# Performance work log

Hardware: AMD Instinct MI355X
Metric: run time of the kernel (lower is better)

Reference implementation:

```python
import jax, jax.numpy as jnp
import numpy as np

N_NODES = 100_000
N_EDGES = 1_600_000
NEG_SLOPE = 0.2

# layer configs: (in_channels, heads, out_channels, has_proj)
LAYERS = [(193, 8, 16, True), (128, 8, 16, False), (128, 8, 16, False), (128, 8, 8, True)]


def _gat_params(key, fin, H, C):
    ks = jax.random.split(key, 6)
    s = 1.0 / np.sqrt(fin)
    Wl = jax.random.normal(ks[0], (fin, H * C), dtype=jnp.float32) * s
    bl = jax.random.normal(ks[1], (H * C,), dtype=jnp.float32) * 0.01
    Wr = jax.random.normal(ks[2], (fin, H * C), dtype=jnp.float32) * s
    br = jax.random.normal(ks[3], (H * C,), dtype=jnp.float32) * 0.01
    att = jax.random.normal(ks[4], (H, C), dtype=jnp.float32) * (1.0 / np.sqrt(C))
    bias = jax.random.normal(ks[5], (H * C,), dtype=jnp.float32) * 0.01
    return Wl, bl, Wr, br, att, bias


def setup_inputs() -> dict:
    key = jax.random.key(0)
    ks = jax.random.split(key, 16)
    inp = {}
    inp['x'] = jax.random.normal(ks[0], (N_NODES, 193), dtype=jnp.float32)
    inp['edge_index'] = jax.random.randint(ks[1], (2, N_EDGES), 0, N_NODES, dtype=jnp.int64)
    for li, (fin, H, C, _) in enumerate(LAYERS, start=1):
        Wl, bl, Wr, br, att, bias = _gat_params(ks[1 + li], fin, H, C)
        inp[f'Wl{li}'] = Wl; inp[f'bl{li}'] = bl
        inp[f'Wr{li}'] = Wr; inp[f'br{li}'] = br
        inp[f'att{li}'] = att; inp[f'bias{li}'] = bias
    # residual projections where in_channels != heads*out_channels
    inp['proj1_W'] = jax.random.normal(ks[8], (193, 128), dtype=jnp.float32) * (1.0 / np.sqrt(193))
    inp['proj1_b'] = jax.random.normal(ks[9], (128,), dtype=jnp.float32) * 0.01
    inp['proj4_W'] = jax.random.normal(ks[10], (128, 64), dtype=jnp.float32) * (1.0 / np.sqrt(128))
    inp['proj4_b'] = jax.random.normal(ks[11], (64,), dtype=jnp.float32) * 0.01
    inp['lin1_W'] = jax.random.normal(ks[12], (64, 32), dtype=jnp.float32) * (1.0 / np.sqrt(64))
    inp['lin1_b'] = jax.random.normal(ks[13], (32,), dtype=jnp.float32) * 0.01
    return inp


def _gatv2(x, src, dst, Wl, bl, Wr, br, att, bias):
    # x: [N, Fin]; att: [H, C]
    N = x.shape[0]
    H, C = att.shape
    xl = (x @ Wl + bl).reshape(N, H, C)  # source transform
    xr = (x @ Wr + br).reshape(N, H, C)  # destination transform
    m = xl[src] + xr[dst]                # [E, H, C] edge gather
    e = jnp.einsum('ehc,hc->eh', jax.nn.leaky_relu(m, NEG_SLOPE), att)  # [E, H]
    emax = jax.ops.segment_max(e, dst, num_segments=N)  # per-dst softmax max
    p = jnp.exp(e - emax[dst])
    denom = jax.ops.segment_sum(p, dst, num_segments=N)
    alpha = p / (denom[dst] + 1e-16)     # [E, H]
    out = jax.ops.segment_sum(alpha[:, :, None] * xl[src], dst, num_segments=N)  # [N, H, C]
    return out.reshape(N, H * C) + bias


def _forward(x, edge_index, params):
    src, dst = edge_index[0], edge_index[1]
    h = x
    for li in range(4):
        Wl, bl, Wr, br, att, bias, projW, projb = params[li]
        g = _gatv2(h, src, dst, Wl, bl, Wr, br, att, bias)
        res = h @ projW + projb if projW is not None else h
        h = jax.nn.gelu(g + res, approximate=False)
    Wf, bf = params[4]
    return h @ Wf + bf


def reference(x, edge_index,
              Wl1, bl1, Wr1, br1, att1, bias1,
              Wl2, bl2, Wr2, br2, att2, bias2,
              Wl3, bl3, Wr3, br3, att3, bias3,
              Wl4, bl4, Wr4, br4, att4, bias4,
              proj1_W, proj1_b, proj4_W, proj4_b, lin1_W, lin1_b):
    params = [
        (Wl1, bl1, Wr1, br1, att1, bias1, proj1_W, proj1_b),
        (Wl2, bl2, Wr2, br2, att2, bias2, None, None),
        (Wl3, bl3, Wr3, br3, att3, bias3, None, None),
        (Wl4, bl4, Wr4, br4, att4, bias4, proj4_W, proj4_b),
        (lin1_W, lin1_b),
    ]
    return _forward(x, edge_index, params)
```

## Files before the change

kernel.cpp:

```cpp
#include <hip/hip_runtime.h>
#include <hip/hip_bf16.h>

#define NNODES 100000

typedef short s16x8 __attribute__((ext_vector_type(8)));
typedef float f32x4 __attribute__((ext_vector_type(4)));

__device__ inline ushort f2bf(float f) {
    uint u = __float_as_uint(f);
    uint r = u + 0x7fffu + ((u >> 16) & 1u);
    return (ushort)(r >> 16);
}
__device__ inline float bf2f(ushort u) { return __uint_as_float(((uint)u) << 16); }
__device__ inline float bflo(uint u) { return __uint_as_float(u << 16); }
__device__ inline float bfhi(uint u) { return __uint_as_float(u & 0xffff0000u); }

__device__ inline void gl_lds16(const ushort* g, ushort* l) {
    __builtin_amdgcn_global_load_lds((const __attribute__((address_space(1))) void*)g,
                                     (__attribute__((address_space(3))) void*)l, 16, 0, 0);
}

__global__ void hist_kernel(const int* __restrict__ dst, int E, int* __restrict__ deg) {
    int e = blockIdx.x * blockDim.x + threadIdx.x;
    if (e < E) atomicAdd(&deg[dst[e]], 1);
}

__global__ __launch_bounds__(256) void scan_part(const int* __restrict__ deg,
                                                 int* __restrict__ bsum, int n) {
    int t = threadIdx.x;
    int base = blockIdx.x * 1024 + t * 4;
    int4 v = make_int4(0, 0, 0, 0);
    if (base + 3 < n) v = *(const int4*)(deg + base);
    else {
        if (base + 0 < n) v.x = deg[base + 0];
        if (base + 1 < n) v.y = deg[base + 1];
        if (base + 2 < n) v.z = deg[base + 2];
    }
    int s = v.x + v.y + v.z + v.w;
#pragma unroll
    for (int o = 1; o < 64; o <<= 1) s += __shfl_xor(s, o);
    __shared__ int ws[4];
    if ((t & 63) == 0) ws[t >> 6] = s;
    __syncthreads();
    if (t == 0) bsum[blockIdx.x] = ws[0] + ws[1] + ws[2] + ws[3];
}

__global__ __launch_bounds__(128) void scan_bsum(int* __restrict__ bsum, int nb,
                                                 int* __restrict__ rowptr, int n) {
    __shared__ int s[128];
    int t = threadIdx.x;
    int v = (t < nb) ? bsum[t] : 0;
    s[t] = v;
    __syncthreads();
#pragma unroll
    for (int o = 1; o < 128; o <<= 1) {
        int u = (t >= o) ? s[t - o] : 0;
        __syncthreads();
        s[t] += u;
        __syncthreads();
    }
    if (t < nb) bsum[t] = s[t] - v;
    if (t == 127) rowptr[n] = s[127];
}

__global__ __launch_bounds__(256) void scan_apply(const int* __restrict__ deg,
                                                  const int* __restrict__ bsum,
                                                  int* __restrict__ rowptr, int n) {
    int t = threadIdx.x;
    int base = blockIdx.x * 1024 + t * 4;
    int4 v = make_int4(0, 0, 0, 0);
    if (base + 3 < n) v = *(const int4*)(deg + base);
    else {
        if (base + 0 < n) v.x = deg[base + 0];
        if (base + 1 < n) v.y = deg[base + 1];
        if (base + 2 < n) v.z = deg[base + 2];
    }
    int s = v.x + v.y + v.z + v.w;
    int lane = t & 63, w = t >> 6;
    int incl = s;
#pragma unroll
    for (int o = 1; o < 64; o <<= 1) {
        int u = __shfl_up(incl, o);
        if (lane >= o) incl += u;
    }
    __shared__ int wsum[4];
    if (lane == 63) wsum[w] = incl;
    __syncthreads();
    int woff = 0;
    if (w > 0) woff += wsum[0];
    if (w > 1) woff += wsum[1];
    if (w > 2) woff += wsum[2];
    int off = bsum[blockIdx.x] + woff + (incl - s);
    int4 r;
    r.x = off;
    r.y = off + v.x;
    r.z = r.y + v.y;
    r.w = r.z + v.z;
    if (base + 3 < n) *(int4*)(rowptr + base) = r;
    else {
        if (base + 0 < n) rowptr[base + 0] = r.x;
        if (base + 1 < n) rowptr[base + 1] = r.y;
        if (base + 2 < n) rowptr[base + 2] = r.z;
    }
}

__global__ void scatter_kernel(const int* __restrict__ src, const int* __restrict__ dst, int E,
                               const int* __restrict__ rowptr, int* __restrict__ cursor,
                               int* __restrict__ csr) {
    int e = blockIdx.x * blockDim.x + threadIdx.x;
    if (e < E) {
        int d = dst[e];
        int pos = rowptr[d] + atomicAdd(&cursor[d], 1);
        csr[pos] = src[e];
    }
}

struct WConvDesc { const float* W; ushort* Wt; int K, N, Kp; };
struct WConvArgs { WConvDesc d[10]; };

__global__ void convert_weights(WConvArgs args) {
    WConvDesc dd = args.d[blockIdx.y];
    int total = dd.N * dd.Kp;
    for (int i = blockIdx.x * 256 + threadIdx.x; i < total; i += gridDim.x * 256) {
        int n = i / dd.Kp, k = i - n * dd.Kp;
        float v = (k < dd.K) ? dd.W[(size_t)k * dd.N + n] : 0.f;
        dd.Wt[i] = f2bf(v);
    }
}

struct BCat { const float* src; float* dst; int len; };
struct BCatArgs { BCat d[10]; };
__global__ void concat_bias(BCatArgs a) {
    BCat dd = a.d[blockIdx.x];
    for (int i = threadIdx.x; i < dd.len; i += 256) dd.dst[i] = dd.src[i];
}

__global__ void convert_x(const float* __restrict__ x, ushort* __restrict__ xb, int M) {
    int total = M * 56;
    for (int i = blockIdx.x * 256 + threadIdx.x; i < total; i += gridDim.x * 256) {
        int n = i / 56;
        int k4 = (i - n * 56) * 4;
        ushort o[4];
#pragma unroll
        for (int j = 0; j < 4; ++j) {
            int k = k4 + j;
            o[j] = (k < 193) ? f2bf(x[(size_t)n * 193 + k]) : (ushort)0;
        }
        *(uint2*)(xb + (size_t)n * 224 + k4) = *(const uint2*)o;
    }
}

template <int BN>
__global__ __launch_bounds__(256) void gemm_mfma(const ushort* __restrict__ A,
                                                 const ushort* __restrict__ BtAll,
                                                 const float* __restrict__ biasAll,
                                                 ushort* __restrict__ C,
                                                 int M, int Kp, int Cstride) {
    const int col0 = blockIdx.y * BN;
    const ushort* Bt = BtAll + (size_t)col0 * Kp;
    const float* bias = biasAll + col0;

    __shared__ ushort As[128 * 32];
    __shared__ ushort Bs[BN * 32];
    const int t = threadIdx.x;
    const int r0 = blockIdx.x * 128;
    const int lane = t & 63;
    const int w = t >> 6;
    const int la = lane & 15;
    const int lk = (lane >> 4) * 8;

    constexpr int MR = (BN == 128) ? 4 : 2;
    const int m0 = (BN == 128) ? (w >> 1) * 64 : w * 32;
    const int n0 = (BN == 128) ? (w & 1) * 64 : 0;

    f32x4 acc[MR][4];
#pragma unroll
    for (int i = 0; i < MR; ++i)
#pragma unroll
        for (int j = 0; j < 4; ++j) acc[i][j] = (f32x4)0.f;

    const int lrow4 = lane >> 2;
    const int lkq = (lane & 3) * 8;
    const int arow0 = min(r0 + (2 * w) * 16 + lrow4, M - 1);
    const int arow1 = min(r0 + (2 * w + 1) * 16 + lrow4, M - 1);
    const size_t aoff0 = (size_t)arow0 * Kp + lkq;
    const size_t aoff1 = (size_t)arow1 * Kp + lkq;
    const int brow0 = (BN == 128) ? (2 * w) * 16 + lrow4 : w * 16 + lrow4;
    const int brow1 = (2 * w + 1) * 16 + lrow4;
    const size_t boff0 = (size_t)brow0 * Kp + lkq;
    const size_t boff1 = (size_t)brow1 * Kp + lkq;

    for (int k0 = 0; k0 < Kp; k0 += 32) {
        gl_lds16(A + aoff0 + k0, &As[(2 * w) * 512]);
        gl_lds16(A + aoff1 + k0, &As[(2 * w + 1) * 512]);
        if (BN == 128) {
            gl_lds16(Bt + boff0 + k0, &Bs[(2 * w) * 512]);
            gl_lds16(Bt + boff1 + k0, &Bs[(2 * w + 1) * 512]);
        } else {
            gl_lds16(Bt + boff0 + k0, &Bs[w * 512]);
        }
        asm volatile("s_waitcnt vmcnt(0)" ::: "memory");
        __syncthreads();
        s16x8 av[MR], bv[4];
#pragma unroll
        for (int i = 0; i < MR; ++i)
            av[i] = *(const s16x8*)&As[(m0 + i * 16 + la) * 32 + lk];
#pragma unroll
        for (int j = 0; j < 4; ++j)
            bv[j] = *(const s16x8*)&Bs[(n0 + j * 16 + la) * 32 + lk];
#pragma unroll
        for (int i = 0; i < MR; ++i)
#pragma unroll
            for (int j = 0; j < 4; ++j)
                acc[i][j] = __builtin_amdgcn_mfma_f32_16x16x32_bf16(av[i], bv[j], acc[i][j], 0, 0, 0);
        __syncthreads();
    }
    const int lrow = (lane >> 4) * 4;
#pragma unroll
    for (int i = 0; i < MR; ++i) {
#pragma unroll
        for (int j = 0; j < 4; ++j) {
            int col = n0 + j * 16 + la;
            float bval = bias[col];
#pragma unroll
            for (int r = 0; r < 4; ++r) {
                int row = r0 + m0 + i * 16 + lrow + r;
                if (row < M) C[(size_t)row * Cstride + col0 + col] = f2bf(acc[i][j][r] + bval);
            }
        }
    }
}

template <int HC>
__global__ __launch_bounds__(256) void gat_agg(const ushort* __restrict__ xcat, int xstride,
                                               int xr_off,
                                               const ushort* __restrict__ res, int rstride, int roff,
                                               const float* __restrict__ att,
                                               const float* __restrict__ bias,
                                               const int* __restrict__ rowptr,
                                               const int* __restrict__ csr,
                                               float* __restrict__ hout, int hstride,
                                               ushort* __restrict__ houtb, int M) {
    constexpr int LPE = HC / 8;
    constexpr int EPI = 64 / LPE;
    constexpr int QSH = (HC == 128) ? 4 : 3;
    const int n = blockIdx.x * 4 + (threadIdx.x >> 6);
    if (n >= M) return;
    const int lane = threadIdx.x & 63;
    const int clane = lane & (LPE - 1);
    const int q = lane >> QSH;

    const char* xb = (const char*)xcat;
    const uint xrowB = (uint)xstride * 2u;
    const uint chB = (uint)clane * 16u;

    float xr[8], at[8];
    {
        uint4 u = *(const uint4*)(xb + (uint)n * xrowB + (uint)xr_off * 2u + chB);
        xr[0] = bflo(u.x); xr[1] = bfhi(u.x); xr[2] = bflo(u.y); xr[3] = bfhi(u.y);
        xr[4] = bflo(u.z); xr[5] = bfhi(u.z); xr[6] = bflo(u.w); xr[7] = bfhi(u.w);
        const float L2E = 1.4426950408889634f;
        float4 a0 = *(const float4*)(att + 8 * clane);
        float4 a1 = *(const float4*)(att + 8 * clane + 4);
        at[0] = a0.x * L2E; at[1] = a0.y * L2E; at[2] = a0.z * L2E; at[3] = a0.w * L2E;
        at[4] = a1.x * L2E; at[5] = a1.y * L2E; at[6] = a1.z * L2E; at[7] = a1.w * L2E;
    }

    const int s0 = rowptr[n], s1 = rowptr[n + 1];
    float ssum = 0.f;
    float acc[8] = {0.f, 0.f, 0.f, 0.f, 0.f, 0.f, 0.f, 0.f};

    if (s1 > s0) {
        const int nq = (s1 - s0 + EPI - 1) >> (6 - QSH);
        auto ISSUE = [&](uint4& buf, bool& val, int p) {
            if (p >= nq) { val = false; buf = make_uint4(0u, 0u, 0u, 0u); return; }
            int g = s0 + p * EPI + q;
            val = g < s1;
            int src = csr[min(g, s1 - 1)];
            buf = *(const uint4*)(xb + (uint)src * xrowB + chB);
        };
        auto COMPUTE = [&](const uint4& buf, bool val) {
            float x[8];
            x[0] = bflo(buf.x); x[1] = bfhi(buf.x); x[2] = bflo(buf.y); x[3] = bfhi(buf.y);
            x[4] = bflo(buf.z); x[5] = bfhi(buf.z); x[6] = bflo(buf.w); x[7] = bfhi(buf.w);
            float prod = 0.f;
#pragma unroll
            for (int j = 0; j < 8; ++j) {
                float v = x[j] + xr[j];
                float l = fmaxf(v, 0.2f * v);
                prod = fmaf(l, at[j], prod);
            }
            if constexpr (HC == 128) prod += __shfl_xor(prod, 1);
            float pe = val ? exp2f(prod) : 0.f;
            ssum += pe;
#pragma unroll
            for (int j = 0; j < 8; ++j) acc[j] = fmaf(pe, x[j], acc[j]);
        };
        uint4 b0, b1, b2, b3;
        bool v0, v1, v2, v3;
        ISSUE(b0, v0, 0); ISSUE(b1, v1, 1); ISSUE(b2, v2, 2); ISSUE(b3, v3, 3);
        for (int p = 0; p < nq; p += 4) {
            COMPUTE(b0, v0); ISSUE(b0, v0, p + 4);
            if (p + 1 < nq) { COMPUTE(b1, v1); ISSUE(b1, v1, p + 5); }
            if (p + 2 < nq) { COMPUTE(b2, v2); ISSUE(b2, v2, p + 6); }
            if (p + 3 < nq) { COMPUTE(b3, v3); ISSUE(b3, v3, p + 7); }
        }
    }

#pragma unroll
    for (int o = LPE; o < 64; o <<= 1) {
        ssum += __shfl_xor(ssum, o);
#pragma unroll
        for (int j = 0; j < 8; ++j) acc[j] += __shfl_xor(acc[j], o);
    }

    float inv = 1.f / (ssum + 1e-16f);
    if constexpr (HC == 128) {
        int ch = 8 * clane + 2 * q;
        float a0s = (q == 0) ? acc[0] : (q == 1) ? acc[2] : (q == 2) ? acc[4] : acc[6];
        float a1s = (q == 0) ? acc[1] : (q == 1) ? acc[3] : (q == 2) ? acc[5] : acc[7];
        uint u = *(const uint*)(res + (size_t)n * rstride + roff + ch);
        float r0v = bflo(u), r1v = bfhi(u);
        float2 b2 = *(const float2*)(bias + ch);
        float y0 = fmaf(a0s, inv, b2.x + r0v);
        float y1 = fmaf(a1s, inv, b2.y + r1v);
        float o0 = 0.5f * y0 * (1.f + erff(y0 * 0.70710678118654752f));
        float o1 = 0.5f * y1 * (1.f + erff(y1 * 0.70710678118654752f));
        if (hout) *(float2*)(hout + (size_t)n * hstride + ch) = make_float2(o0, o1);
        if (houtb) *(uint*)(houtb + (size_t)n * HC + ch) = (uint)f2bf(o0) | ((uint)f2bf(o1) << 16);
    } else {
        int ch = 8 * clane + q;
        float a0s = (q == 0) ? acc[0] : (q == 1) ? acc[1] : (q == 2) ? acc[2] : (q == 3) ? acc[3]
                  : (q == 4) ? acc[4] : (q == 5) ? acc[5] : (q == 6) ? acc[6] : acc[7];
        float r0v = bf2f(res[(size_t)n * rstride + roff + ch]);
        float y0 = fmaf(a0s, inv, bias[ch] + r0v);
        float o0 = 0.5f * y0 * (1.f + erff(y0 * 0.70710678118654752f));
        if (hout) hout[(size_t)n * hstride + ch] = o0;
        if (houtb) houtb[(size_t)n * HC + ch] = f2bf(o0);
    }
}

__global__ __launch_bounds__(256) void final_linear(const float* __restrict__ h,
                                                    const float* __restrict__ W,
                                                    const float* __restrict__ b,
                                                    float* __restrict__ out, int M) {
    __shared__ float Ws[64 * 32];
    __shared__ float bs[32];
    __shared__ float hs[8][64];
    int t = threadIdx.x;
    for (int i = t; i < 64 * 32; i += 256) Ws[i] = W[i];
    if (t < 32) bs[t] = b[t];
    int r0 = blockIdx.x * 8;
    for (int i = t; i < 8 * 64; i += 256) {
        int r = i >> 6, c = i & 63;
        hs[r][c] = (r0 + r < M) ? h[(size_t)(r0 + r) * 64 + c] : 0.f;
    }
    __syncthreads();
    int lr = t >> 5;
    int col = t & 31;
    int row = r0 + lr;
    if (row >= M) return;
    float acc = bs[col];
#pragma unroll 8
    for (int k = 0; k < 64; ++k) acc += hs[lr][k] * Ws[k * 32 + col];
    out[(size_t)row * 32 + col] = acc;
}

extern "C" void kernel_launch(void* const* d_in, const int* in_sizes, int n_in,
                              void* d_out, int out_size, void* d_ws, size_t ws_size,
                              hipStream_t stream) {
    const float* x = (const float*)d_in[0];
    const int* ei = (const int*)d_in[1];
    const int E = in_sizes[1] / 2;
    const int* srcp = ei;
    const int* dstp = ei + E;

    const float* Wl[4]  = {(const float*)d_in[2],  (const float*)d_in[8],  (const float*)d_in[14], (const float*)d_in[20]};
    const float* bl[4]  = {(const float*)d_in[3],  (const float*)d_in[9],  (const float*)d_in[15], (const float*)d_in[21]};
    const float* Wr[4]  = {(const float*)d_in[4],  (const float*)d_in[10], (const float*)d_in[16], (const float*)d_in[22]};
    const float* br[4]  = {(const float*)d_in[5],  (const float*)d_in[11], (const float*)d_in[17], (const float*)d_in[23]};
    const float* att[4] = {(const float*)d_in[6],  (const float*)d_in[12], (const float*)d_in[18], (const float*)d_in[24]};
    const float* bia[4] = {(const float*)d_in[7],  (const float*)d_in[13], (const float*)d_in[19], (const float*)d_in[25]};
    const float* proj1W = (const float*)d_in[26];
    const float* proj1b = (const float*)d_in[27];
    const float* proj4W = (const float*)d_in[28];
    const float* proj4b = (const float*)d_in[29];
    const float* linW   = (const float*)d_in[30];
    const float* linb   = (const float*)d_in[31];

    const int M = NNODES;
    ushort* xcat = (ushort*)d_ws;
    ushort* xb   = xcat + (size_t)M * 384;
    ushort* hb1  = xb;
    ushort* hb2  = xb + (size_t)M * 224;
    float* h4 = (float*)(hb2 + (size_t)M * 128);
    ushort* wb = (ushort*)(h4 + (size_t)M * 64);
    ushort* WtC1 = wb; wb += 384 * 224;
    ushort* WtC2 = wb; wb += 256 * 128;
    ushort* WtC3 = wb; wb += 256 * 128;
    ushort* WtC4 = wb; wb += 192 * 128;
    float* bc1 = (float*)wb;
    float* bc2 = bc1 + 384;
    float* bc3 = bc2 + 256;
    float* bc4 = bc3 + 256;
    int* deg    = (int*)(bc4 + 192);
    int* cursor = deg + M;
    int* rowptr = cursor + M;
    int* csr    = rowptr + (M + 1);
    int* bsum   = csr + E;

    const int NB = (M + 1023) / 1024;

    hipMemsetAsync(deg, 0, 2 * (size_t)M * sizeof(int), stream);
    hist_kernel<<<(E + 255) / 256, 256, 0, stream>>>(dstp, E, deg);
    scan_part<<<NB, 256, 0, stream>>>(deg, bsum, M);
    scan_bsum<<<1, 128, 0, stream>>>(bsum, NB, rowptr, M);
    scan_apply<<<NB, 256, 0, stream>>>(deg, bsum, rowptr, M);
    scatter_kernel<<<(E + 255) / 256, 256, 0, stream>>>(srcp, dstp, E, rowptr, cursor, csr);

    WConvArgs wa;
    wa.d[0] = {Wl[0],  WtC1,             193, 128, 224};
    wa.d[1] = {Wr[0],  WtC1 + 128 * 224, 193, 128, 224};
    wa.d[2] = {proj1W, WtC1 + 256 * 224, 193, 128, 224};
    wa.d[3] = {Wl[1],  WtC2,             128, 128, 128};
    wa.d[4] = {Wr[1],  WtC2 + 128 * 128, 128, 128, 128};
    wa.d[5] = {Wl[2],  WtC3,             128, 128, 128};
    wa.d[6] = {Wr[2],  WtC3 + 128 * 128, 128, 128, 128};
    wa.d[7] = {Wl[3],  WtC4,             128, 64, 128};
    wa.d[8] = {Wr[3],  WtC4 + 64 * 128,  128, 64, 128};
    wa.d[9] = {proj4W, WtC4 + 128 * 128, 128, 64, 128};
    convert_weights<<<dim3(112, 10), 256, 0, stream>>>(wa);
    BCatArgs ba;
    ba.d[0] = {bl[0],  bc1,       128};
    ba.d[1] = {br[0],  bc1 + 128, 128};
    ba.d[2] = {proj1b, bc1 + 256, 128};
    ba.d[3] = {bl[1],  bc2,       128};
    ba.d[4] = {br[1],  bc2 + 128, 128};
    ba.d[5] = {bl[2],  bc3,       128};
    ba.d[6] = {br[2],  bc3 + 128, 128};
    ba.d[7] = {bl[3],  bc4,       64};
    ba.d[8] = {br[3],  bc4 + 64,  64};
    ba.d[9] = {proj4b, bc4 + 128, 64};
    concat_bias<<<10, 256, 0, stream>>>(ba);
    convert_x<<<2048, 256, 0, stream>>>(x, xb, M);

    const int GX = (M + 127) / 128;
    dim3 ag((M + 3) / 4, 1);

    gemm_mfma<128><<<dim3(GX, 3), 256, 0, stream>>>(xb, WtC1, bc1, xcat, M, 224, 384);
    gat_agg<128><<<ag, 256, 0, stream>>>(xcat, 384, 128, xcat, 384, 256, att[0], bia[0],
                                         rowptr, csr, nullptr, 0, hb1, M);
    gemm_mfma<128><<<dim3(GX, 2), 256, 0, stream>>>(hb1, WtC2, bc2, xcat, M, 128, 256);
    gat_agg<128><<<ag, 256, 0, stream>>>(xcat, 256, 128, hb1, 128, 0, att[1], bia[1],
                                         rowptr, csr, nullptr, 0, hb2, M);
    gemm_mfma<128><<<dim3(GX, 2), 256, 0, stream>>>(hb2, WtC3, bc3, xcat, M, 128, 256);
    gat_agg<128><<<ag, 256, 0, stream>>>(xcat, 256, 128, hb2, 128, 0, att[2], bia[2],
                                         rowptr, csr, nullptr, 0, hb1, M);
    gemm_mfma<64><<<dim3(GX, 3), 256, 0, stream>>>(hb1, WtC4, bc4, xcat, M, 128, 192);
    gat_agg<64><<<ag, 256, 0, stream>>>(xcat, 192, 64, xcat, 192, 128, att[3], bia[3],
                                        rowptr, csr, h4, 64, nullptr, M);
    final_linear<<<(M + 7) / 8, 256, 0, stream>>>(h4, linW, linb, (float*)d_out, M);
}
```

Baseline: 672.1 us.

## Fuse final linear into last GAT aggregation and remap GEMM blocks per XCD

Folds the final 64x32 linear layer into the layer-4 aggregation kernel, so the fp32 h4 intermediate is no longer written to and reread from global memory and one launch is dropped. Each wave computes its node's output from LDS-staged weights. GEMM blocks are also relaid onto a 1D grid so that all column panels of a row tile land on the same XCD, which is meant to improve L2 reuse of the A tile. The costs are extra LDS weight loading in every aggregation block and a few idle padding blocks in the GEMM grid.

```diff
diff --git a/kernel.cpp b/kernel.cpp
--- a/kernel.cpp
+++ b/kernel.cpp
@@ -155,15 +155,22 @@
                                                  const ushort* __restrict__ BtAll,
                                                  const float* __restrict__ biasAll,
                                                  ushort* __restrict__ C,
-                                                 int M, int Kp, int Cstride) {
-    const int col0 = blockIdx.y * BN;
+                                                 int M, int Kp, int Cstride,
+                                                 int GX, int NPAN) {
+    const int id = blockIdx.x;
+    const int xcd = id & 7;
+    const int j = id >> 3;
+    const int y = j % NPAN;
+    const int xblk = (j / NPAN) * 8 + xcd;
+    if (xblk >= GX) return;
+    const int r0 = xblk * 128;
+    const int col0 = y * BN;
     const ushort* Bt = BtAll + (size_t)col0 * Kp;
     const float* bias = biasAll + col0;
 
     __shared__ ushort As[128 * 32];
     __shared__ ushort Bs[BN * 32];
     const int t = threadIdx.x;
-    const int r0 = blockIdx.x * 128;
     const int lane = t & 63;
     const int w = t >> 6;
     const int la = lane & 15;
@@ -177,7 +184,7 @@
 #pragma unroll
     for (int i = 0; i < MR; ++i)
 #pragma unroll
-        for (int j = 0; j < 4; ++j) acc[i][j] = (f32x4)0.f;
+        for (int j2 = 0; j2 < 4; ++j2) acc[i][j2] = (f32x4)0.f;
 
     const int lrow4 = lane >> 2;
     const int lkq = (lane & 3) * 8;
@@ -206,49 +213,44 @@
         for (int i = 0; i < MR; ++i)
             av[i] = *(const s16x8*)&As[(m0 + i * 16 + la) * 32 + lk];
 #pragma unroll
-        for (int j = 0; j < 4; ++j)
-            bv[j] = *(const s16x8*)&Bs[(n0 + j * 16 + la) * 32 + lk];
+        for (int j2 = 0; j2 < 4; ++j2)
+            bv[j2] = *(const s16x8*)&Bs[(n0 + j2 * 16 + la) * 32 + lk];
 #pragma unroll
         for (int i = 0; i < MR; ++i)
 #pragma unroll
-            for (int j = 0; j < 4; ++j)
-                acc[i][j] = __builtin_amdgcn_mfma_f32_16x16x32_bf16(av[i], bv[j], acc[i][j], 0, 0, 0);
+            for (int j2 = 0; j2 < 4; ++j2)
+                acc[i][j2] = __builtin_amdgcn_mfma_f32_16x16x32_bf16(av[i], bv[j2], acc[i][j2], 0, 0, 0);
         __syncthreads();
     }
     const int lrow = (lane >> 4) * 4;
 #pragma unroll
     for (int i = 0; i < MR; ++i) {
 #pragma unroll
-        for (int j = 0; j < 4; ++j) {
-            int col = n0 + j * 16 + la;
+        for (int j2 = 0; j2 < 4; ++j2) {
+            int col = n0 + j2 * 16 + la;
             float bval = bias[col];
 #pragma unroll
             for (int r = 0; r < 4; ++r) {
                 int row = r0 + m0 + i * 16 + lrow + r;
-                if (row < M) C[(size_t)row * Cstride + col0 + col] = f2bf(acc[i][j][r] + bval);
+                if (row < M) C[(size_t)row * Cstride + col0 + col] = f2bf(acc[i][j2][r] + bval);
             }
         }
     }
 }
 
-template <int HC>
-__global__ __launch_bounds__(256) void gat_agg(const ushort* __restrict__ xcat, int xstride,
-                                               int xr_off,
-                                               const ushort* __restrict__ res, int rstride, int roff,
-                                               const float* __restrict__ att,
-                                               const float* __restrict__ bias,
-                                               const int* __restrict__ rowptr,
-                                               const int* __restrict__ csr,
-                                               float* __restrict__ hout, int hstride,
-                                               ushort* __restrict__ houtb, int M) {
-    constexpr int LPE = HC / 8;
-    constexpr int EPI = 64 / LPE;
-    constexpr int QSH = (HC == 128) ? 4 : 3;
+__global__ __launch_bounds__(256) void gat_agg128(const ushort* __restrict__ xcat, int xstride,
+                                                  int xr_off,
+                                                  const ushort* __restrict__ res, int rstride, int roff,
+                                                  const float* __restrict__ att,
+                                                  const float* __restrict__ bias,
+                                                  const int* __restrict__ rowptr,
+                                                  const int* __restrict__ csr,
+                                                  ushort* __restrict__ houtb, int M) {
     const int n = blockIdx.x * 4 + (threadIdx.x >> 6);
     if (n >= M) return;
     const int lane = threadIdx.x & 63;
-    const int clane = lane & (LPE - 1);
-    const int q = lane >> QSH;
+    const int clane = lane & 15;
+    const int q = lane >> 4;
 
     const char* xb = (const char*)xcat;
     const uint xrowB = (uint)xstride * 2u;
@@ -271,10 +273,10 @@
     float acc[8] = {0.f, 0.f, 0.f, 0.f, 0.f, 0.f, 0.f, 0.f};
 
     if (s1 > s0) {
-        const int nq = (s1 - s0 + EPI - 1) >> (6 - QSH);
+        const int nq = (s1 - s0 + 3) >> 2;
         auto ISSUE = [&](uint4& buf, bool& val, int p) {
             if (p >= nq) { val = false; buf = make_uint4(0u, 0u, 0u, 0u); return; }
-            int g = s0 + p * EPI + q;
+            int g = s0 + p * 4 + q;
             val = g < s1;
             int src = csr[min(g, s1 - 1)];
             buf = *(const uint4*)(xb + (uint)src * xrowB + chB);
@@ -290,7 +292,7 @@
                 float l = fmaxf(v, 0.2f * v);
                 prod = fmaf(l, at[j], prod);
             }
-            if constexpr (HC == 128) prod += __shfl_xor(prod, 1);
+            prod += __shfl_xor(prod, 1);
             float pe = val ? exp2f(prod) : 0.f;
             ssum += pe;
 #pragma unroll
@@ -308,62 +310,134 @@
     }
 
 #pragma unroll
-    for (int o = LPE; o < 64; o <<= 1) {
+    for (int o = 16; o < 64; o <<= 1) {
         ssum += __shfl_xor(ssum, o);
 #pragma unroll
         for (int j = 0; j < 8; ++j) acc[j] += __shfl_xor(acc[j], o);
     }
 
     float inv = 1.f / (ssum + 1e-16f);
-    if constexpr (HC == 128) {
-        int ch = 8 * clane + 2 * q;
-        float a0s = (q == 0) ? acc[0] : (q == 1) ? acc[2] : (q == 2) ? acc[4] : acc[6];
-        float a1s = (q == 0) ? acc[1] : (q == 1) ? acc[3] : (q == 2) ? acc[5] : acc[7];
-        uint u = *(const uint*)(res + (size_t)n * rstride + roff + ch);
-        float r0v = bflo(u), r1v = bfhi(u);
-        float2 b2 = *(const float2*)(bias + ch);
-        float y0 = fmaf(a0s, inv, b2.x + r0v);
-        float y1 = fmaf(a1s, inv, b2.y + r1v);
-        float o0 = 0.5f * y0 * (1.f + erff(y0 * 0.70710678118654752f));
-        float o1 = 0.5f * y1 * (1.f + erff(y1 * 0.70710678118654752f));
-        if (hout) *(float2*)(hout + (size_t)n * hstride + ch) = make_float2(o0, o1);
-        if (houtb) *(uint*)(houtb + (size_t)n * HC + ch) = (uint)f2bf(o0) | ((uint)f2bf(o1) << 16);
-    } else {
-        int ch = 8 * clane + q;
-        float a0s = (q == 0) ? acc[0] : (q == 1) ? acc[1] : (q == 2) ? acc[2] : (q == 3) ? acc[3]
-                  : (q == 4) ? acc[4] : (q == 5) ? acc[5] : (q == 6) ? acc[6] : acc[7];
-        float r0v = bf2f(res[(size_t)n * rstride + roff + ch]);
-        float y0 = fmaf(a0s, inv, bias[ch] + r0v);
-        float o0 = 0.5f * y0 * (1.f + erff(y0 * 0.70710678118654752f));
-        if (hout) hout[(size_t)n * hstride + ch] = o0;
-        if (houtb) houtb[(size_t)n * HC + ch] = f2bf(o0);
-    }
-}
-
-__global__ __launch_bounds__(256) void final_linear(const float* __restrict__ h,
-                                                    const float* __restrict__ W,
-                                                    const float* __restrict__ b,
-                                                    float* __restrict__ out, int M) {
+    int ch = 8 * clane + 2 * q;
+    float a0s = (q == 0) ? acc[0] : (q == 1) ? acc[2] : (q == 2) ? acc[4] : acc[6];
+    float a1s = (q == 0) ? acc[1] : (q == 1) ? acc[3] : (q == 2) ? acc[5] : acc[7];
+    uint u = *(const uint*)(res + (size_t)n * rstride + roff + ch);
+    float r0v = bflo(u), r1v = bfhi(u);
+    float2 b2 = *(const float2*)(bias + ch);
+    float y0 = fmaf(a0s, inv, b2.x + r0v);
+    float y1 = fmaf(a1s, inv, b2.y + r1v);
+    float o0 = 0.5f * y0 * (1.f + erff(y0 * 0.70710678118654752f));
+    float o1 = 0.5f * y1 * (1.f + erff(y1 * 0.70710678118654752f));
+    *(uint*)(houtb + (size_t)n * 128 + ch) = (uint)f2bf(o0) | ((uint)f2bf(o1) << 16);
+}
+
+__global__ __launch_bounds__(256) void gat_agg64_lin(const ushort* __restrict__ xcat, int xstride,
+                                                     int xr_off,
+                                                     const ushort* __restrict__ res, int rstride, int roff,
+                                                     const float* __restrict__ att,
+                                                     const float* __restrict__ bias,
+                                                     const int* __restrict__ rowptr,
+                                                     const int* __restrict__ csr,
+                                                     const float* __restrict__ linW,
+                                                     const float* __restrict__ linb,
+                                                     float* __restrict__ out, int M) {
     __shared__ float Ws[64 * 32];
-    __shared__ float bs[32];
-    __shared__ float hs[8][64];
-    int t = threadIdx.x;
-    for (int i = t; i < 64 * 32; i += 256) Ws[i] = W[i];
-    if (t < 32) bs[t] = b[t];
-    int r0 = blockIdx.x * 8;
-    for (int i = t; i < 8 * 64; i += 256) {
-        int r = i >> 6, c = i & 63;
-        hs[r][c] = (r0 + r < M) ? h[(size_t)(r0 + r) * 64 + c] : 0.f;
+    __shared__ float hs[4][64];
+    {
+        int t = threadIdx.x;
+#pragma unroll
+        for (int i = 0; i < 8; ++i) Ws[t + 256 * i] = linW[t + 256 * i];
     }
     __syncthreads();
-    int lr = t >> 5;
-    int col = t & 31;
-    int row = r0 + lr;
-    if (row >= M) return;
-    float acc = bs[col];
-#pragma unroll 8
-    for (int k = 0; k < 64; ++k) acc += hs[lr][k] * Ws[k * 32 + col];
-    out[(size_t)row * 32 + col] = acc;
+
+    const int wid = threadIdx.x >> 6;
+    const int n = blockIdx.x * 4 + wid;
+    if (n >= M) return;
+    const int lane = threadIdx.x & 63;
+    const int clane = lane & 7;
+    const int q = lane >> 3;
+
+    const char* xb = (const char*)xcat;
+    const uint xrowB = (uint)xstride * 2u;
+    const uint chB = (uint)clane * 16u;
+
+    float xr[8], at[8];
+    {
+        uint4 u = *(const uint4*)(xb + (uint)n * xrowB + (uint)xr_off * 2u + chB);
+        xr[0] = bflo(u.x); xr[1] = bfhi(u.x); xr[2] = bflo(u.y); xr[3] = bfhi(u.y);
+        xr[4] = bflo(u.z); xr[5] = bfhi(u.z); xr[6] = bflo(u.w); xr[7] = bfhi(u.w);
+        const float L2E = 1.4426950408889634f;
+        float4 a0 = *(const float4*)(att + 8 * clane);
+        float4 a1 = *(const float4*)(att + 8 * clane + 4);
+        at[0] = a0.x * L2E; at[1] = a0.y * L2E; at[2] = a0.z * L2E; at[3] = a0.w * L2E;
+        at[4] = a1.x * L2E; at[5] = a1.y * L2E; at[6] = a1.z * L2E; at[7] = a1.w * L2E;
+    }
+
+    const int s0 = rowptr[n], s1 = rowptr[n + 1];
+    float ssum = 0.f;
+    float acc[8] = {0.f, 0.f, 0.f, 0.f, 0.f, 0.f, 0.f, 0.f};
+
+    if (s1 > s0) {
+        const int nq = (s1 - s0 + 7) >> 3;
+        auto ISSUE = [&](uint4& buf, bool& val, int p) {
+            if (p >= nq) { val = false; buf = make_uint4(0u, 0u, 0u, 0u); return; }
+            int g = s0 + p * 8 + q;
+            val = g < s1;
+            int src = csr[min(g, s1 - 1)];
+            buf = *(const uint4*)(xb + (uint)src * xrowB + chB);
+        };
+        auto COMPUTE = [&](const uint4& buf, bool val) {
+            float x[8];
+            x[0] = bflo(buf.x); x[1] = bfhi(buf.x); x[2] = bflo(buf.y); x[3] = bfhi(buf.y);
+            x[4] = bflo(buf.z); x[5] = bfhi(buf.z); x[6] = bflo(buf.w); x[7] = bfhi(buf.w);
+            float prod = 0.f;
+#pragma unroll
+            for (int j = 0; j < 8; ++j) {
+                float v = x[j] + xr[j];
+                float l = fmaxf(v, 0.2f * v);
+                prod = fmaf(l, at[j], prod);
+            }
+            float pe = val ? exp2f(prod) : 0.f;
+            ssum += pe;
+#pragma unroll
+            for (int j = 0; j < 8; ++j) acc[j] = fmaf(pe, x[j], acc[j]);
+        };
+        uint4 b0, b1, b2, b3;
+        bool v0, v1, v2, v3;
+        ISSUE(b0, v0, 0); ISSUE(b1, v1, 1); ISSUE(b2, v2, 2); ISSUE(b3, v3, 3);
+        for (int p = 0; p < nq; p += 4) {
+            COMPUTE(b0, v0); ISSUE(b0, v0, p + 4);
+            if (p + 1 < nq) { COMPUTE(b1, v1); ISSUE(b1, v1, p + 5); }
+            if (p + 2 < nq) { COMPUTE(b2, v2); ISSUE(b2, v2, p + 6); }
+            if (p + 3 < nq) { COMPUTE(b3, v3); ISSUE(b3, v3, p + 7); }
+        }
+    }
+
+#pragma unroll
+    for (int o = 8; o < 64; o <<= 1) {
+        ssum += __shfl_xor(ssum, o);
+#pragma unroll
+        for (int j = 0; j < 8; ++j) acc[j] += __shfl_xor(acc[j], o);
+    }
+
+    float inv = 1.f / (ssum + 1e-16f);
+    int ch = 8 * clane + q;
+    float a0s = (q == 0) ? acc[0] : (q == 1) ? acc[1] : (q == 2) ? acc[2] : (q == 3) ? acc[3]
+              : (q == 4) ? acc[4] : (q == 5) ? acc[5] : (q == 6) ? acc[6] : acc[7];
+    float r0v = bf2f(res[(size_t)n * rstride + roff + ch]);
+    float y0 = fmaf(a0s, inv, bias[ch] + r0v);
+    float o0 = 0.5f * y0 * (1.f + erff(y0 * 0.70710678118654752f));
+
+    hs[wid][ch] = o0;
+    asm volatile("s_waitcnt lgkmcnt(0)" ::: "memory");
+    const int col = lane & 31;
+    const int half = lane >> 5;
+    const float* hp = &hs[wid][half * 32];
+    const float* wp = &Ws[(half * 32) * 32 + col];
+    float a = 0.f;
+#pragma unroll
+    for (int k = 0; k < 32; ++k) a = fmaf(hp[k], wp[k * 32], a);
+    a += __shfl_xor(a, 32);
+    if (half == 0) out[(size_t)n * 32 + col] = a + linb[col];
 }
 
 extern "C" void kernel_launch(void* const* d_in, const int* in_sizes, int n_in,
@@ -393,8 +467,7 @@
     ushort* xb   = xcat + (size_t)M * 384;
     ushort* hb1  = xb;
     ushort* hb2  = xb + (size_t)M * 224;
-    float* h4 = (float*)(hb2 + (size_t)M * 128);
-    ushort* wb = (ushort*)(h4 + (size_t)M * 64);
+    ushort* wb = hb2 + (size_t)M * 128;
     ushort* WtC1 = wb; wb += 384 * 224;
     ushort* WtC2 = wb; wb += 256 * 128;
     ushort* WtC3 = wb; wb += 256 * 128;
@@ -445,19 +518,19 @@
     convert_x<<<2048, 256, 0, stream>>>(x, xb, M);
 
     const int GX = (M + 127) / 128;
+    const int S8 = ((GX + 7) / 8) * 8;
     dim3 ag((M + 3) / 4, 1);
 
-    gemm_mfma<128><<<dim3(GX, 3), 256, 0, stream>>>(xb, WtC1, bc1, xcat, M, 224, 384);
-    gat_agg<128><<<ag, 256, 0, stream>>>(xcat, 384, 128, xcat, 384, 256, att[0], bia[0],
-                                         rowptr, csr, nullptr, 0, hb1, M);
-    gemm_mfma<128><<<dim3(GX, 2), 256, 0, stream>>>(hb1, WtC2, bc2, xcat, M, 128, 256);
-    gat_agg<128><<<ag, 256, 0, stream>>>(xcat, 256, 128, hb1, 128, 0, att[1], bia[1],
-                                         rowptr, csr, nullptr, 0, hb2, M);
-    gemm_mfma<128><<<dim3(GX, 2), 256, 0, stream>>>(hb2, WtC3, bc3, xcat, M, 128, 256);
-    gat_agg<128><<<ag, 256, 0, stream>>>(xcat, 256, 128, hb2, 128, 0, att[2], bia[2],
-                                         rowptr, csr, nullptr, 0, hb1, M);
-    gemm_mfma<64><<<dim3(GX, 3), 256, 0, stream>>>(hb1, WtC4, bc4, xcat, M, 128, 192);
-    gat_agg<64><<<ag, 256, 0, stream>>>(xcat, 192, 64, xcat, 192, 128, att[3], bia[3],
-                                        rowptr, csr, h4, 64, nullptr, M);
-    final_linear<<<(M + 7) / 8, 256, 0, stream>>>(h4, linW, linb, (float*)d_out, M);
-}
+    gemm_mfma<128><<<S8 * 3, 256, 0, stream>>>(xb, WtC1, bc1, xcat, M, 224, 384, GX, 3);
+    gat_agg128<<<ag, 256, 0, stream>>>(xcat, 384, 128, xcat, 384, 256, att[0], bia[0],
+                                       rowptr, csr, hb1, M);
+    gemm_mfma<128><<<S8 * 2, 256, 0, stream>>>(hb1, WtC2, bc2, xcat, M, 128, 256, GX, 2);
+    gat_agg128<<<ag, 256, 0, stream>>>(xcat, 256, 128, hb1, 128, 0, att[1], bia[1],
+                                       rowptr, csr, hb2, M);
+    gemm_mfma<128><<<S8 * 2, 256, 0, stream>>>(hb2, WtC3, bc3, xcat, M, 128, 256, GX, 2);
+    gat_agg128<<<ag, 256, 0, stream>>>(xcat, 256, 128, hb2, 128, 0, att[2], bia[2],
+                                       rowptr, csr, hb1, M);
+    gemm_mfma<64><<<S8 * 3, 256, 0, stream>>>(hb1, WtC4, bc4, xcat, M, 128, 192, GX, 3);
+    gat_agg64_lin<<<ag, 256, 0, stream>>>(xcat, 192, 64, xcat, 192, 128, att[3], bia[3],
+                                          rowptr, csr, linW, linb, (float*)d_out, M);
+}
```

New measurement: 659.4 us. No clear change (-1.9%).
